# Kernel optimization log

Hardware: AMD Instinct MI355X
Metric: run time of the kernel (lower is better)

## Reference

```python
import jax, jax.numpy as jnp
import numpy as np


def setup_inputs() -> dict:
    key = jax.random.key(0)
    ks = jax.random.split(key, 8)
    B, S, H, I = 2, 1025, 3200, 12800
    T = B * S
    # int8 tensors represented as int32, symmetric range [-128, 126]
    hidden_states = jax.random.randint(ks[0], (B, S, H), 0, 255, dtype=jnp.int32) - 127
    scale_in = (jax.random.uniform(ks[1], (T,)) * 0.02 + 1e-4).astype(jnp.float16)
    w1 = jax.random.randint(ks[2], (I, H), 0, 255, dtype=jnp.int32) - 127
    w1_scale = (jax.random.uniform(ks[3], (I,)) * 0.01 + 1e-4).astype(jnp.float32)
    b1 = (jax.random.normal(ks[4], (I,)) * 0.02).astype(jnp.float16)
    w2 = jax.random.randint(ks[5], (H, I), 0, 255, dtype=jnp.int32) - 127
    w2_scale = (jax.random.uniform(ks[6], (H,)) * 0.01 + 1e-4).astype(jnp.float32)
    b2 = (jax.random.normal(ks[7], (H,)) * 0.02).astype(jnp.float16)
    return {"hidden_states": hidden_states, "scale_in": scale_in,
            "w1": w1, "w1_scale": w1_scale, "b1": b1,
            "w2": w2, "w2_scale": w2_scale, "b2": b2}


def _w8a8_linear(x_int, scale_x, w_int, w_scale, bias):
    # int8 GEMM with int32 accumulation, dequant with per-token * per-channel scales
    acc = jnp.matmul(x_int, w_int.T)  # [T, out] int32
    out = acc.astype(jnp.float32) * scale_x[:, None].astype(jnp.float32) * w_scale[None, :]
    return (out + bias.astype(jnp.float32)).astype(jnp.float16)


def _gelu_and_quant(x_f16):
    # fused GELU + per-token dynamic symmetric int8 quantization
    g = jax.nn.gelu(x_f16.astype(jnp.float32), approximate=False)  # [T, I]
    amax = jnp.max(jnp.abs(g), axis=-1)                              # [T]
    scale_act = (amax / 127.0).astype(jnp.float16)
    s = jnp.maximum(scale_act.astype(jnp.float32), 1e-8)
    q = jnp.clip(jnp.round(g / s[:, None]), -128, 127).astype(jnp.int32)
    return q, scale_act


def reference(hidden_states, scale_in, w1, w1_scale, b1, w2, w2_scale, b2):
    B, S, H = hidden_states.shape
    x = hidden_states.reshape(-1, H)               # [T, H] int
    fc1_out = _w8a8_linear(x, scale_in, w1, w1_scale, b1)      # [T, I] fp16
    act_out, scale_act = _gelu_and_quant(fc1_out)              # int8-as-int32, [T] fp16
    fc2_out = _w8a8_linear(act_out, scale_act, w2, w2_scale, b2)  # [T, H] fp16
    return fc2_out
```

## Files before the change

kernel.cpp:

```cpp
#include <hip/hip_runtime.h>
#include <hip/hip_fp16.h>

typedef int v4i __attribute__((ext_vector_type(4)));

#define AS1C(p) ((const __attribute__((address_space(1))) void*)(p))
#define AS3(p)  ((__attribute__((address_space(3))) void*)(p))

__launch_bounds__(1024, 4)
__global__ void gemm256(const signed char* __restrict__ A, const signed char* __restrict__ Bw,
                        int M, int N, int K,
                        const float* __restrict__ scale_tok, const float* __restrict__ wsc,
                        const float* __restrict__ bias,
                        __half* __restrict__ gout, unsigned int* __restrict__ amax) {
  __shared__ __align__(16) char smem[2][32768];
  const int tid = threadIdx.x;
  const int lane = tid & 63, wave = tid >> 6;
  const int wavem = wave >> 2, waven = wave & 3;
  const int lh = lane & 15, sseg = lane >> 4;

  const int gy = gridDim.y;
  int lid;
  {
    const int o = blockIdx.y * gridDim.x + blockIdx.x;
    const int nwg = gridDim.x * gy;
    const int q = nwg >> 3, r = nwg & 7;
    const int x = o & 7, p = o >> 3;
    lid = (x < r ? x * (q + 1) : r * (q + 1) + (x - r) * q) + p;
  }
  const long long t0 = (long long)(lid % gy) * 256;
  const long long n0 = (long long)(lid / gy) * 256;
  const int nk = K >> 6;
  const long long Mm1 = M - 1, Nm1 = N - 1;

  const int lr4 = lane >> 2, slot = lane & 3;
  const int rloc = wave * 16 + lr4;
  const int gslot = (slot ^ ((rloc >> 1) & 3)) << 4;
  const signed char* sp0;
  const signed char* sp1;
  {
    long long gr = t0 + rloc; if (gr > Mm1) gr = Mm1;
    sp0 = A + gr * (long long)K + gslot;
    long long gn = n0 + rloc; if (gn > Nm1) gn = Nm1;
    sp1 = Bw + gn * (long long)K + gslot;
  }
  const int d0 = wave * 1024, d1 = 16384 + wave * 1024;

#define STAGE(bi) do { \
    __builtin_amdgcn_global_load_lds(AS1C(sp0), AS3(&smem[bi][d0]), 16, 0, 0); sp0 += 64; \
    __builtin_amdgcn_global_load_lds(AS1C(sp1), AS3(&smem[bi][d1]), 16, 0, 0); sp1 += 64; \
  } while (0)

  const int xs = ((sseg ^ ((lh >> 1) & 3)) << 4);
  const int offA = wavem * 4096 + lh * 64 + xs;
  const int offB = 16384 + waven * 4096 + lh * 64 + xs;

  v4i acc[4][4] = {};

  STAGE(0);
  __syncthreads();

  int cur = 0;
  for (int kt = 0; kt < nk; ++kt) {
    if (kt + 1 < nk) STAGE(cur ^ 1);
    const char* base = smem[cur];
    v4i af[4], bf[2];
#pragma unroll
    for (int mi = 0; mi < 4; ++mi) af[mi] = *(const v4i*)(base + offA + mi * 1024);
    bf[0] = *(const v4i*)(base + offB);
    bf[1] = *(const v4i*)(base + offB + 1024);
#pragma unroll
    for (int mi = 0; mi < 4; ++mi) {
      acc[mi][0] = __builtin_amdgcn_mfma_i32_16x16x64_i8(af[mi], bf[0], acc[mi][0], 0, 0, 0);
      acc[mi][1] = __builtin_amdgcn_mfma_i32_16x16x64_i8(af[mi], bf[1], acc[mi][1], 0, 0, 0);
    }
    bf[0] = *(const v4i*)(base + offB + 2048);
    bf[1] = *(const v4i*)(base + offB + 3072);
#pragma unroll
    for (int mi = 0; mi < 4; ++mi) {
      acc[mi][2] = __builtin_amdgcn_mfma_i32_16x16x64_i8(af[mi], bf[0], acc[mi][2], 0, 0, 0);
      acc[mi][3] = __builtin_amdgcn_mfma_i32_16x16x64_i8(af[mi], bf[1], acc[mi][3], 0, 0, 0);
    }
    __syncthreads();
    cur ^= 1;
  }
#undef STAGE

  long long cidx[4]; float w4[4], bi4[4]; bool cok[4];
#pragma unroll
  for (int ni = 0; ni < 4; ++ni) {
    cidx[ni] = n0 + waven * 64 + ni * 16 + lh;
    cok[ni] = cidx[ni] < N;
    w4[ni] = cok[ni] ? wsc[cidx[ni]] : 0.f;
    bi4[ni] = cok[ni] ? bias[cidx[ni]] : 0.f;
  }
#pragma unroll
  for (int mi = 0; mi < 4; ++mi) {
#pragma unroll
    for (int j = 0; j < 4; ++j) {
      const long long t = t0 + wavem * 64 + mi * 16 + (lane >> 4) * 4 + j;
      const bool valid = t < M;
      const float st = valid ? scale_tok[t] : 0.f;
      float rowmax = 0.f;
#pragma unroll
      for (int ni = 0; ni < 4; ++ni) {
        float v = (float)acc[mi][ni][j] * st * w4[ni] + bi4[ni];
        v = __half2float(__float2half(v));
        const float gl = 0.5f * v * (1.f + erff(v * 0.70710678118654752f));
        rowmax = fmaxf(rowmax, fabsf(gl));
        if (valid && cok[ni]) gout[t * (long long)N + cidx[ni]] = __float2half(gl);
      }
#pragma unroll
      for (int m = 1; m < 16; m <<= 1) rowmax = fmaxf(rowmax, __shfl_xor(rowmax, m));
      if (valid && lh == 0) atomicMax(&amax[t], __float_as_uint(rowmax));
    }
  }
}

__device__ __forceinline__ void stage_tile(const signed char* __restrict__ g, long long ld,
                                           long long rmax, long long r0, int k0,
                                           char* lds, int tid) {
  const int wave = tid >> 6, lane = tid & 63;
#pragma unroll
  for (int p = 0; p < 2; ++p) {
    const int chunk = wave * 2 + p;
    const int row = chunk * 16 + (lane >> 2);
    const int slot = lane & 3;
    const int gslot = slot ^ ((row >> 1) & 3);
    long long rg = r0 + row;
    if (rg > rmax) rg = rmax;
    const signed char* src = g + rg * ld + (long long)k0 + gslot * 16;
    char* dst = lds + chunk * 1024;
    __builtin_amdgcn_global_load_lds(AS1C(src), AS3(dst), 16, 0, 0);
  }
}

__launch_bounds__(256, 4)
__global__ void gemm_fc2(const signed char* __restrict__ A, const signed char* __restrict__ Bw,
                         int M, int N, int K,
                         const float* __restrict__ wsc, const float* __restrict__ bias,
                         unsigned int* __restrict__ amax, float* __restrict__ fout) {
  __shared__ __align__(16) char lds[2][2][128 * 64];
  const int tid = threadIdx.x;
  const int lane = tid & 63, wave = tid >> 6;
  const int wrow = (wave >> 1) * 64, wcol = (wave & 1) * 64;

  const int gy = gridDim.y;
  int lid;
  {
    const int o = blockIdx.y * gridDim.x + blockIdx.x;
    const int nwg = gridDim.x * gy;
    const int q = nwg >> 3, r = nwg & 7;
    const int x = o & 7, p = o >> 3;
    lid = (x < r ? x * (q + 1) : r * (q + 1) + (x - r) * q) + p;
  }
  const long long t0 = (long long)(lid % gy) * 128;
  const long long n0 = (long long)(lid / gy) * 128;

  v4i acc[4][4] = {};

  stage_tile(A, K, (long long)M - 1, t0, 0, lds[0][0], tid);
  stage_tile(Bw, K, (long long)N - 1, n0, 0, lds[0][1], tid);
  __syncthreads();

  const int nk = K >> 6;
  int cur = 0;
  const int srow = lane & 15, sseg = lane >> 4;
  for (int kt = 0; kt < nk; ++kt) {
    if (kt + 1 < nk) {
      stage_tile(A, K, (long long)M - 1, t0, (kt + 1) << 6, lds[cur ^ 1][0], tid);
      stage_tile(Bw, K, (long long)N - 1, n0, (kt + 1) << 6, lds[cur ^ 1][1], tid);
    }
    v4i af[4], bf[4];
#pragma unroll
    for (int mi = 0; mi < 4; ++mi) {
      const int r = wrow + mi * 16 + srow;
      const int sl = sseg ^ ((r >> 1) & 3);
      af[mi] = *(const v4i*)&lds[cur][0][r * 64 + sl * 16];
    }
#pragma unroll
    for (int ni = 0; ni < 4; ++ni) {
      const int r = wcol + ni * 16 + srow;
      const int sl = sseg ^ ((r >> 1) & 3);
      bf[ni] = *(const v4i*)&lds[cur][1][r * 64 + sl * 16];
    }
#pragma unroll
    for (int mi = 0; mi < 4; ++mi)
#pragma unroll
      for (int ni = 0; ni < 4; ++ni)
        acc[mi][ni] = __builtin_amdgcn_mfma_i32_16x16x64_i8(af[mi], bf[ni], acc[mi][ni], 0, 0, 0);
    __syncthreads();
    cur ^= 1;
  }

#pragma unroll
  for (int mi = 0; mi < 4; ++mi) {
#pragma unroll
    for (int j = 0; j < 4; ++j) {
      const long long t = t0 + wrow + mi * 16 + (lane >> 4) * 4 + j;
      if (t < M) {
        const float am = __uint_as_float(amax[t]);
        const float st = __half2float(__float2half(am * (1.f / 127.f)));
#pragma unroll
        for (int ni = 0; ni < 4; ++ni) {
          const long long c = n0 + wcol + ni * 16 + (lane & 15);
          const float v = (float)acc[mi][ni][j] * st * wsc[c] + bias[c];
          fout[t * (long long)N + c] = __half2float(__float2half(v));
        }
      }
    }
  }
}

__global__ void pack_all(const int* __restrict__ a, const int* __restrict__ b,
                         const int* __restrict__ c,
                         signed char* __restrict__ pa, signed char* __restrict__ pb,
                         signed char* __restrict__ pc,
                         unsigned int* __restrict__ amax,
                         long long na, long long nb, long long nc, int T) {
  const long long gid = blockIdx.x * (long long)blockDim.x + threadIdx.x;
  if (gid < T) amax[gid] = 0u;
  const long long n4a = na >> 2, n4b = nb >> 2, n4c = nc >> 2;
  const long long tot = n4a + n4b + n4c;
  const long long stride = (long long)gridDim.x * blockDim.x;
  for (long long u = gid; u < tot; u += stride) {
    const int* src; signed char* dst; long long loc;
    if (u < n4a)            { src = a; dst = pa; loc = u; }
    else if (u < n4a + n4b) { src = b; dst = pb; loc = u - n4a; }
    else                    { src = c; dst = pc; loc = u - n4a - n4b; }
    const int4 v = *(const int4*)(src + (loc << 2));
    const unsigned out = (unsigned)(v.x & 0xff) | ((unsigned)(v.y & 0xff) << 8) |
                         ((unsigned)(v.z & 0xff) << 16) | ((unsigned)(v.w & 0xff) << 24);
    *(unsigned*)(dst + (loc << 2)) = out;
  }
}

__global__ void gelu_quant(const __half* __restrict__ g, const unsigned int* __restrict__ amax,
                           signed char* __restrict__ q, long long total, int I) {
  const long long nchunk = total >> 3;
  const long long stride = (long long)gridDim.x * blockDim.x;
  for (long long c = blockIdx.x * (long long)blockDim.x + threadIdx.x; c < nchunk; c += stride) {
    const long long base = c << 3;
    const int t = (int)(base / I);
    const float am = __uint_as_float(amax[t]);
    const float s = fmaxf(__half2float(__float2half(am * (1.f / 127.f))), 1e-8f);
    const float inv = 1.f / s;
    const int4 raw = *(const int4*)(g + base);
    const __half2* h2 = (const __half2*)&raw;
    union { signed char b[8]; int2 v; } u;
#pragma unroll
    for (int k = 0; k < 4; ++k) {
      const float2 f = __half22float2(h2[k]);
      const float q0 = fminf(fmaxf(rintf(f.x * inv), -128.f), 127.f);
      const float q1 = fminf(fmaxf(rintf(f.y * inv), -128.f), 127.f);
      u.b[k * 2]     = (signed char)(int)q0;
      u.b[k * 2 + 1] = (signed char)(int)q1;
    }
    *(int2*)(q + base) = u.v;
  }
}

extern "C" void kernel_launch(void* const* d_in, const int* in_sizes, int n_in,
                              void* d_out, int out_size, void* d_ws, size_t ws_size,
                              hipStream_t stream) {
  const int* hs = (const int*)d_in[0];
  const float* scale_in = (const float*)d_in[1];
  const int* w1 = (const int*)d_in[2];
  const float* w1s = (const float*)d_in[3];
  const float* b1 = (const float*)d_in[4];
  const int* w2 = (const int*)d_in[5];
  const float* w2s = (const float*)d_in[6];
  const float* b2 = (const float*)d_in[7];

  const int T = in_sizes[1];
  const int I = in_sizes[3];
  const int H = in_sizes[6];

  char* ws = (char*)d_ws;
  unsigned int* amax = (unsigned int*)ws;
  signed char* px  = (signed char*)(ws + 16384);
  signed char* pw1 = px + (size_t)T * H;
  signed char* pw2 = pw1 + (size_t)I * H;
  __half* gbuf = (__half*)(pw2 + (size_t)H * I);
  signed char* qbuf = (signed char*)(gbuf + (size_t)T * I);

  const long long nx = (long long)T * H, nw1 = (long long)I * H, nw2 = (long long)H * I;

  pack_all<<<2048, 256, 0, stream>>>(hs, w1, w2, px, pw1, pw2, amax, nx, nw1, nw2, T);

  dim3 g1(I / 256, (T + 255) / 256);
  gemm256<<<g1, 1024, 0, stream>>>(px, pw1, T, I, H, scale_in, w1s, b1, gbuf, amax);

  gelu_quant<<<2048, 256, 0, stream>>>(gbuf, amax, qbuf, (long long)T * I, I);

  dim3 g2(H / 128, (T + 127) / 128);
  gemm_fc2<<<g2, 256, 0, stream>>>(qbuf, pw2, T, H, I, w2s, b2, amax, (float*)d_out);
}
```

Measured before the change: 374.7 us.

## Overlap w2 int8 packing with fc1 GEMM via extra pack blocks

Moves the w2 int32-to-int8 packing out of the initial pack kernel and into the fc1 GEMM launch, where the first 128 workgroups pack w2 and the rest run the GEMM. The GEMM is flattened to a 1D grid with remapped tile ids. The intent is to hide the memory-bound w2 conversion behind the compute-bound fc1 GEMM and shorten the serial pack phase. The risk is that pack blocks compete for bandwidth and CU slots, and the 1024-thread pack blocks may finish unevenly.

Result: faster. 366.3 us (-2.3%).

```diff
diff --git a/kernel.cpp b/kernel.cpp
--- a/kernel.cpp
+++ b/kernel.cpp
@@ -6,23 +6,57 @@
 #define AS1C(p) ((const __attribute__((address_space(1))) void*)(p))
 #define AS3(p)  ((__attribute__((address_space(3))) void*)(p))
 
+__global__ void pack1(const int* __restrict__ a, const int* __restrict__ b,
+                      signed char* __restrict__ pa, signed char* __restrict__ pb,
+                      unsigned int* __restrict__ amax,
+                      long long na, long long nb, int T) {
+  const long long gid = blockIdx.x * (long long)blockDim.x + threadIdx.x;
+  if (gid < T) amax[gid] = 0u;
+  const long long n4a = na >> 2, n4b = nb >> 2;
+  const long long tot = n4a + n4b;
+  const long long stride = (long long)gridDim.x * blockDim.x;
+  for (long long u = gid; u < tot; u += stride) {
+    const int* src; signed char* dst; long long loc;
+    if (u < n4a) { src = a; dst = pa; loc = u; }
+    else         { src = b; dst = pb; loc = u - n4a; }
+    const int4 v = *(const int4*)(src + (loc << 2));
+    const unsigned out = (unsigned)(v.x & 0xff) | ((unsigned)(v.y & 0xff) << 8) |
+                         ((unsigned)(v.z & 0xff) << 16) | ((unsigned)(v.w & 0xff) << 24);
+    *(unsigned*)(dst + (loc << 2)) = out;
+  }
+}
+
 __launch_bounds__(1024, 4)
-__global__ void gemm256(const signed char* __restrict__ A, const signed char* __restrict__ Bw,
-                        int M, int N, int K,
-                        const float* __restrict__ scale_tok, const float* __restrict__ wsc,
-                        const float* __restrict__ bias,
-                        __half* __restrict__ gout, unsigned int* __restrict__ amax) {
+__global__ void fc1_fused(const signed char* __restrict__ A, const signed char* __restrict__ Bw,
+                          int M, int N, int K,
+                          const float* __restrict__ scale_tok, const float* __restrict__ wsc,
+                          const float* __restrict__ bias,
+                          __half* __restrict__ gout, unsigned int* __restrict__ amax,
+                          const int* __restrict__ w2src, signed char* __restrict__ w2dst,
+                          long long n4w2, int npack, int gy) {
   __shared__ __align__(16) char smem[2][32768];
+  const int bid = blockIdx.x;
+
+  if (bid < npack) {
+    const long long stride = (long long)npack * 1024;
+    for (long long u = (long long)bid * 1024 + threadIdx.x; u < n4w2; u += stride) {
+      const int4 v = *(const int4*)(w2src + (u << 2));
+      const unsigned out = (unsigned)(v.x & 0xff) | ((unsigned)(v.y & 0xff) << 8) |
+                           ((unsigned)(v.z & 0xff) << 16) | ((unsigned)(v.w & 0xff) << 24);
+      *(unsigned*)(w2dst + (u << 2)) = out;
+    }
+    return;
+  }
+
   const int tid = threadIdx.x;
   const int lane = tid & 63, wave = tid >> 6;
   const int wavem = wave >> 2, waven = wave & 3;
   const int lh = lane & 15, sseg = lane >> 4;
 
-  const int gy = gridDim.y;
   int lid;
   {
-    const int o = blockIdx.y * gridDim.x + blockIdx.x;
-    const int nwg = gridDim.x * gy;
+    const int o = bid - npack;
+    const int nwg = gridDim.x - npack;
     const int q = nwg >> 3, r = nwg & 7;
     const int x = o & 7, p = o >> 3;
     lid = (x < r ? x * (q + 1) : r * (q + 1) + (x - r) * q) + p;
@@ -208,29 +242,6 @@
         }
       }
     }
-  }
-}
-
-__global__ void pack_all(const int* __restrict__ a, const int* __restrict__ b,
-                         const int* __restrict__ c,
-                         signed char* __restrict__ pa, signed char* __restrict__ pb,
-                         signed char* __restrict__ pc,
-                         unsigned int* __restrict__ amax,
-                         long long na, long long nb, long long nc, int T) {
-  const long long gid = blockIdx.x * (long long)blockDim.x + threadIdx.x;
-  if (gid < T) amax[gid] = 0u;
-  const long long n4a = na >> 2, n4b = nb >> 2, n4c = nc >> 2;
-  const long long tot = n4a + n4b + n4c;
-  const long long stride = (long long)gridDim.x * blockDim.x;
-  for (long long u = gid; u < tot; u += stride) {
-    const int* src; signed char* dst; long long loc;
-    if (u < n4a)            { src = a; dst = pa; loc = u; }
-    else if (u < n4a + n4b) { src = b; dst = pb; loc = u - n4a; }
-    else                    { src = c; dst = pc; loc = u - n4a - n4b; }
-    const int4 v = *(const int4*)(src + (loc << 2));
-    const unsigned out = (unsigned)(v.x & 0xff) | ((unsigned)(v.y & 0xff) << 8) |
-                         ((unsigned)(v.z & 0xff) << 16) | ((unsigned)(v.w & 0xff) << 24);
-    *(unsigned*)(dst + (loc << 2)) = out;
   }
 }
 
@@ -285,10 +296,14 @@
 
   const long long nx = (long long)T * H, nw1 = (long long)I * H, nw2 = (long long)H * I;
 
-  pack_all<<<2048, 256, 0, stream>>>(hs, w1, w2, px, pw1, pw2, amax, nx, nw1, nw2, T);
-
-  dim3 g1(I / 256, (T + 255) / 256);
-  gemm256<<<g1, 1024, 0, stream>>>(px, pw1, T, I, H, scale_in, w1s, b1, gbuf, amax);
+  pack1<<<2048, 256, 0, stream>>>(hs, w1, px, pw1, amax, nx, nw1, T);
+
+  const int NPACK = 128;
+  const int gy1 = (T + 255) / 256;
+  const int gemmBlocks = (I / 256) * gy1;
+  fc1_fused<<<NPACK + gemmBlocks, 1024, 0, stream>>>(
+      px, pw1, T, I, H, scale_in, w1s, b1, gbuf, amax,
+      w2, pw2, nw2 >> 2, NPACK, gy1);
 
   gelu_quant<<<2048, 256, 0, stream>>>(gbuf, amax, qbuf, (long long)T * I, I);
 
```
